# Kernel tuning notes

Hardware: AMD Instinct MI355X
Metric: run time of the kernel (lower is better)

Reference implementation:

```python
import jax, jax.numpy as jnp
import numpy as np
import math

L, B, S, D, H, DI, V = 4, 2, 1024, 768, 12, 3072, 512
DK = D // H

def gelu_tanh(x):
    c = math.sqrt(2.0 / math.pi)
    return 0.5 * x * (1.0 + jnp.tanh(c * (x + 0.044715 * x ** 3)))

def layer_norm(x, g, b, eps=1e-5):
    mu = jnp.mean(x, axis=-1, keepdims=True)
    var = jnp.var(x, axis=-1, keepdims=True)
    return (x - mu) * jax.lax.rsqrt(var + eps) * g + b

def setup_inputs() -> dict:
    key = jax.random.key(0)
    ks = jax.random.split(key, 12)
    w = 0.02  # init scale
    return {
        "x": jax.random.randint(ks[0], (B, S), 0, V),
        "embed": jax.random.normal(ks[1], (V, D), jnp.float32) * w,
        "pos_emb": jax.random.normal(ks[2], (S, D), jnp.float32) * w,
        "ln1_g": jnp.ones((L, D), jnp.float32),
        "ln1_b": jnp.zeros((L, D), jnp.float32),
        "wq": jax.random.normal(ks[3], (L, D, D), jnp.float32) * w,
        "bq": jnp.zeros((L, D), jnp.float32),
        "wk": jax.random.normal(ks[4], (L, D, D), jnp.float32) * w,
        "bk": jnp.zeros((L, D), jnp.float32),
        "wv": jax.random.normal(ks[5], (L, D, D), jnp.float32) * w,
        "bv": jnp.zeros((L, D), jnp.float32),
        "wo": jax.random.normal(ks[6], (L, D, D), jnp.float32) * w,
        "bo": jnp.zeros((L, D), jnp.float32),
        "ln2_g": jnp.ones((L, D), jnp.float32),
        "ln2_b": jnp.zeros((L, D), jnp.float32),
        "w_in": jax.random.normal(ks[7], (L, D, DI), jnp.float32) * w,
        "b_in": jnp.zeros((L, DI), jnp.float32),
        "w_out": jax.random.normal(ks[8], (L, DI, D), jnp.float32) * w,
        "b_out": jnp.zeros((L, D), jnp.float32),
        "lnf_g": jnp.ones((D,), jnp.float32),
        "lnf_b": jnp.zeros((D,), jnp.float32),
        "out_w": jax.random.normal(ks[9], (D, V), jnp.float32) * w,
    }

def reference(x, embed, pos_emb, ln1_g, ln1_b, wq, bq, wk, bk, wv, bv, wo, bo,
              ln2_g, ln2_b, w_in, b_in, w_out, b_out, lnf_g, lnf_b, out_w):
    s = x.shape[1]
    h = embed[x] + pos_emb[None, :s]                       # [B,S,D]
    causal = jnp.tril(jnp.ones((s, s), bool))              # True = keep
    scale = 1.0 / math.sqrt(DK)
    for l in range(L):
        a = layer_norm(h, ln1_g[l], ln1_b[l])
        q = (a @ wq[l] + bq[l]).reshape(-1, s, H, DK)
        k = (a @ wk[l] + bk[l]).reshape(-1, s, H, DK)
        v = (a @ wv[l] + bv[l]).reshape(-1, s, H, DK)
        scores = jnp.einsum('bqhd,bkhd->bhqk', q, k) * scale
        scores = jnp.where(causal, scores, -jnp.inf)
        attn = jax.nn.softmax(scores, axis=-1)
        o = jnp.einsum('bhqk,bkhd->bqhd', attn, v).reshape(-1, s, D)
        h = h + o @ wo[l] + bo[l]
        f = layer_norm(h, ln2_g[l], ln2_b[l])
        h = h + gelu_tanh(f @ w_in[l] + b_in[l]) @ w_out[l] + b_out[l]
    h = layer_norm(h, lnf_g, lnf_b)
    return h @ out_w                                       # [B,S,V] logits
```

## Files before the change

kernel.cpp:

```cpp
#include <hip/hip_runtime.h>
#include <hip/hip_bf16.h>


#define TKN    2048
#define DMODEL 768
#define SEQ    1024
#define NH     12
#define DHEAD  64
#define DFF    3072
#define NL     4
#define NVOCAB 512
#define NQKV   2304

typedef unsigned short u16;
typedef __attribute__((ext_vector_type(4))) float f32x4;
typedef __attribute__((ext_vector_type(8))) short short8;
typedef __attribute__((ext_vector_type(4))) unsigned short us4;

__device__ __forceinline__ u16 f2bf(float f) {
  unsigned u = __builtin_bit_cast(unsigned, f);
  u += 0x7fffu + ((u >> 16) & 1u);
  return (u16)(u >> 16);
}

__device__ __forceinline__ float bf2f(u16 u) {
  unsigned v = ((unsigned)u) << 16;
  return __builtin_bit_cast(float, v);
}

__device__ __forceinline__ short8 mk8(us4 lo, us4 hi) {
  short8 r;
  r[0] = (short)lo[0]; r[1] = (short)lo[1]; r[2] = (short)lo[2]; r[3] = (short)lo[3];
  r[4] = (short)hi[0]; r[5] = (short)hi[1]; r[6] = (short)hi[2]; r[7] = (short)hi[3];
  return r;
}

__device__ __forceinline__ void gload16(const u16* g, u16* l) {
  __builtin_amdgcn_global_load_lds(
      (const __attribute__((address_space(1))) unsigned int*)g,
      (__attribute__((address_space(3))) unsigned int*)l, 16, 0, 0);
}

__global__ __launch_bounds__(256) void k_embed(const int* __restrict__ x,
                                               const float* __restrict__ emb,
                                               const float* __restrict__ pos,
                                               float* __restrict__ h) {
  int t = blockIdx.x;
  int s = t & (SEQ - 1);
  int id = x[t];
  int d = threadIdx.x;
#pragma unroll
  for (int j = 0; j < 3; ++j, d += 256)
    h[t * DMODEL + d] = emb[id * DMODEL + d] + pos[s * DMODEL + d];
}

__global__ __launch_bounds__(256) void k_ln(const float* __restrict__ h,
                                            const float* __restrict__ gam,
                                            const float* __restrict__ bet,
                                            u16* __restrict__ out) {
  __shared__ float sbuf[8];
  int row = blockIdx.x, tid = threadIdx.x;
  const float* hr = h + (size_t)row * DMODEL;
  float x0 = hr[tid], x1 = hr[tid + 256], x2 = hr[tid + 512];
  float s = x0 + x1 + x2;
#pragma unroll
  for (int off = 32; off > 0; off >>= 1) s += __shfl_down(s, off);
  if ((tid & 63) == 0) sbuf[tid >> 6] = s;
  __syncthreads();
  float mu = (sbuf[0] + sbuf[1] + sbuf[2] + sbuf[3]) * (1.0f / DMODEL);
  float d0 = x0 - mu, d1 = x1 - mu, d2 = x2 - mu;
  float v = d0 * d0 + d1 * d1 + d2 * d2;
#pragma unroll
  for (int off = 32; off > 0; off >>= 1) v += __shfl_down(v, off);
  if ((tid & 63) == 0) sbuf[4 + (tid >> 6)] = v;
  __syncthreads();
  float var = (sbuf[4] + sbuf[5] + sbuf[6] + sbuf[7]) * (1.0f / DMODEL);
  float rstd = rsqrtf(var + 1e-5f);
  size_t o = (size_t)row * DMODEL;
  out[o + tid]       = f2bf(d0 * rstd * gam[tid]       + bet[tid]);
  out[o + tid + 256] = f2bf(d1 * rstd * gam[tid + 256] + bet[tid + 256]);
  out[o + tid + 512] = f2bf(d2 * rstd * gam[tid + 512] + bet[tid + 512]);
}

__device__ __forceinline__ void cvt_tile(const float* __restrict__ src, int ldS,
                                         int k0, int n0src,
                                         u16* __restrict__ dst, int ldD, int n0dst,
                                         int tid, u16 (*tl)[72]) {
  int kr = tid >> 2, nj = (tid & 3) << 4;
  const float* sp = src + (size_t)(k0 + kr) * ldS + n0src + nj;
  float4 a0 = ((const float4*)sp)[0];
  float4 a1 = ((const float4*)sp)[1];
  float4 a2 = ((const float4*)sp)[2];
  float4 a3 = ((const float4*)sp)[3];
  u16* tr = &tl[kr][nj];
  tr[0]=f2bf(a0.x); tr[1]=f2bf(a0.y); tr[2]=f2bf(a0.z); tr[3]=f2bf(a0.w);
  tr[4]=f2bf(a1.x); tr[5]=f2bf(a1.y); tr[6]=f2bf(a1.z); tr[7]=f2bf(a1.w);
  tr[8]=f2bf(a2.x); tr[9]=f2bf(a2.y); tr[10]=f2bf(a2.z); tr[11]=f2bf(a2.w);
  tr[12]=f2bf(a3.x); tr[13]=f2bf(a3.y); tr[14]=f2bf(a3.z); tr[15]=f2bf(a3.w);
  __syncthreads();
  int nr = tid >> 2, kj = (tid & 3) << 4;
  us4 o[4];
#pragma unroll
  for (int c = 0; c < 4; ++c)
#pragma unroll
    for (int i = 0; i < 4; ++i) o[c][i] = tl[kj + c * 4 + i][nr];
  u16* dp = dst + (size_t)(n0dst + nr) * ldD + k0 + kj;
  ((us4*)dp)[0] = o[0]; ((us4*)dp)[1] = o[1];
  ((us4*)dp)[2] = o[2]; ((us4*)dp)[3] = o[3];
}

__global__ __launch_bounds__(256) void k_cvtL(const float* __restrict__ wq,
                                              const float* __restrict__ wk,
                                              const float* __restrict__ wv,
                                              const float* __restrict__ wo,
                                              const float* __restrict__ win,
                                              const float* __restrict__ wout,
                                              u16* __restrict__ wqkvT,
                                              u16* __restrict__ woT,
                                              u16* __restrict__ winT,
                                              u16* __restrict__ woutT) {
  __shared__ u16 tl[64][72];
  const int l = blockIdx.y;
  const size_t wDD = (size_t)DMODEL * DMODEL, wDF = (size_t)DMODEL * DFF;
  int t = blockIdx.x, tid = threadIdx.x;
  if (t < 432) {
    int kt = t % 12, ntile = t / 12;
    int gn0 = ntile * 64, sel = gn0 / DMODEL;
    const float* src = (sel == 0 ? wq : sel == 1 ? wk : wv) + l * wDD;
    cvt_tile(src, DMODEL, kt * 64, gn0 - sel * DMODEL,
             wqkvT + l * (size_t)NQKV * DMODEL, DMODEL, gn0, tid, tl);
  } else if (t < 576) {
    int t2 = t - 432, kt = t2 % 12, nt = t2 / 12;
    cvt_tile(wo + l * wDD, DMODEL, kt * 64, nt * 64,
             woT + l * wDD, DMODEL, nt * 64, tid, tl);
  } else if (t < 1152) {
    int t3 = t - 576, kt = t3 % 12, nt = t3 / 12;
    cvt_tile(win + l * wDF, DFF, kt * 64, nt * 64,
             winT + l * wDF, DMODEL, nt * 64, tid, tl);
  } else {
    int t4 = t - 1152, kt = t4 % 48, nt = t4 / 48;
    cvt_tile(wout + l * wDF, DMODEL, kt * 64, nt * 64,
             woutT + l * wDF, DFF, nt * 64, tid, tl);
  }
}

__global__ __launch_bounds__(256) void k_cvtT(const float* __restrict__ src,
                                              u16* __restrict__ dst,
                                              int K, int N) {
  __shared__ u16 tl[64][72];
  cvt_tile(src, N, blockIdx.x * 64, blockIdx.y * 64, dst, K, blockIdx.y * 64,
           threadIdx.x, tl);
}

__global__ __launch_bounds__(256) void k_packb(const float* __restrict__ bq,
                                               const float* __restrict__ bk,
                                               const float* __restrict__ bv,
                                               float* __restrict__ dst) {
  int i = blockIdx.x * 256 + threadIdx.x;
  if (i < NL * NQKV) {
    int l = i / NQKV, j = i - l * NQKV;
    float v = j < DMODEL ? bq[l * DMODEL + j]
            : j < 2 * DMODEL ? bk[l * DMODEL + j - DMODEL]
            : bv[l * DMODEL + j - 2 * DMODEL];
    dst[i] = v;
  }
}

template <int EP, int BM, int BN>
__global__ __launch_bounds__(256) void k_mm(const u16* __restrict__ A,
                                            const u16* __restrict__ BT,
                                            const float* __restrict__ bias,
                                            void* __restrict__ outp,
                                            int N, int K) {
  constexpr int MI = BM / 32;
  constexpr int NJ = BN / 32;
  __shared__ __align__(16) u16 As[2][BM * 64];
  __shared__ __align__(16) u16 Bs[2][BN * 64];
  const int nbx = gridDim.x;
  int lin = blockIdx.y * nbx + blockIdx.x;
  const int chunk = (nbx * gridDim.y) >> 3;
  lin = (lin & 7) * chunk + (lin >> 3);
  const int bn = (lin % nbx) * BN, bm = (lin / nbx) * BM;

  const int tid = threadIdx.x, lane = tid & 63, wid = tid >> 6;
  const int g = lane >> 4, fl = lane & 15;
  const int wm = wid >> 1, wn = wid & 1;

  const int srow = wid * 8 + (lane >> 3);
  const int scol = ((lane & 7) ^ (lane >> 3)) << 3;
  const u16* ag = A + (size_t)(bm + srow) * K + scol;
  const u16* bg = BT + (size_t)(bn + srow) * K + scol;

  f32x4 acc[MI][NJ] = {};
  const int sw = (fl & 7) << 4;

  auto stage = [&](int buf, int kk) {
#pragma unroll
    for (int is = 0; is < MI; ++is)
      gload16(ag + kk + (size_t)is * 32 * K, &As[buf][wid * 512 + is * 2048]);
#pragma unroll
    for (int is = 0; is < NJ; ++is)
      gload16(bg + kk + (size_t)is * 32 * K, &Bs[buf][wid * 512 + is * 2048]);
  };

  const int ks = K / gridDim.z;
  const int kb0 = blockIdx.z * ks;
  const int nk = ks >> 6;
  stage(0, kb0);
  __syncthreads();
  int cur = 0;
  for (int kt = 0; kt < nk; ++kt) {
    if (kt + 1 < nk) stage(cur ^ 1, kb0 + ((kt + 1) << 6));
#pragma unroll
    for (int k0 = 0; k0 < 64; k0 += 32) {
      const int bo = (k0 + 4 * g) * 2;
      short8 af[MI], bf[NJ];
#pragma unroll
      for (int i = 0; i < MI; ++i) {
        const char* base = (const char*)&As[cur][(wm * (BM / 2) + i * 16 + fl) * 64];
        af[i] = mk8(*(const us4*)(base + (bo ^ sw)),
                    *(const us4*)(base + ((bo + 32) ^ sw)));
      }
#pragma unroll
      for (int j = 0; j < NJ; ++j) {
        const char* base = (const char*)&Bs[cur][(wn * (BN / 2) + j * 16 + fl) * 64];
        bf[j] = mk8(*(const us4*)(base + (bo ^ sw)),
                    *(const us4*)(base + ((bo + 32) ^ sw)));
      }
#pragma unroll
      for (int i = 0; i < MI; ++i)
#pragma unroll
        for (int j = 0; j < NJ; ++j)
          acc[i][j] = __builtin_amdgcn_mfma_f32_16x16x32_bf16(af[i], bf[j], acc[i][j], 0, 0, 0);
    }
    __syncthreads();
    cur ^= 1;
  }

  const int row0 = bm + wm * (BM / 2) + 4 * g;
  const int col0 = bn + wn * (BN / 2) + fl;
#pragma unroll
  for (int j = 0; j < NJ; ++j) {
    int col = col0 + j * 16;
    float bv = (EP == 3) ? 0.0f : bias[col];
    if (EP == 1 && blockIdx.z != 0) bv = 0.0f;
#pragma unroll
    for (int i = 0; i < MI; ++i) {
#pragma unroll
      for (int r = 0; r < 4; ++r) {
        int row = row0 + i * 16 + r;
        float val = acc[i][j][r] + bv;
        size_t idx = (size_t)row * N + col;
        if (EP == 0) {
          ((u16*)outp)[idx] = f2bf(val);
        } else if (EP == 1) {
          atomicAdd(&((float*)outp)[idx], val);
        } else if (EP == 2) {
          float t = 0.7978845608028654f * (val + 0.044715f * val * val * val);
          ((u16*)outp)[idx] = f2bf(0.5f * val * (1.0f + tanhf(t)));
        } else if (EP == 3) {
          ((float*)outp)[idx] = val;
        } else {
          int sel = col / DMODEL;
          int c = col - sel * DMODEL;
          int hh2 = c >> 6, dk = c & 63;
          int bb = row >> 10, ss = row & (SEQ - 1);
          if (sel == 0) val *= 0.125f;
          ((u16*)outp)[(size_t)sel * (TKN * DMODEL) +
                       (((size_t)(bb * NH + hh2) * SEQ + ss) << 6) + dk] = f2bf(val);
        }
      }
    }
  }
}

__global__ __launch_bounds__(256) void k_attn(const u16* __restrict__ qh,
                                              u16* __restrict__ pO,
                                              float* __restrict__ pML) {
  __shared__ u16 Vt[DHEAD * 68];
  int bid = blockIdx.x;
  int lin = (bid & 7) * 216 + (bid >> 3);
  const int bh = lin / 72;
  const int idx = lin - bh * 72;
  int qb = 0, sp = 0, c = 0;
#pragma unroll
  for (int q = 0; q < 16; ++q) {
    int n = 1 + (q >> 1);
    if (idx >= c && idx < c + n) { qb = q; sp = idx - c; }
    c += n;
  }
  const int nsp = 1 + (qb >> 1), nt = qb + 1;
  const int t_lo = sp * nt / nsp, t_hi = (sp + 1) * nt / nsp;

  const int b = bh / NH, hh = bh % NH;
  const u16* kh = qh + TKN * DMODEL;
  const u16* vh = qh + 2 * (TKN * DMODEL);
  const size_t headbase = ((size_t)bh * SEQ) << 6;

  const int tid = threadIdx.x, lane = tid & 63, w = tid >> 6;
  const int g = lane >> 4, fl = lane & 15;
  const int qrow = qb * 64 + w * 16 + fl;

  short8 qf[2];
  {
    const u16* qp = qh + headbase + ((size_t)qrow << 6);
#pragma unroll
    for (int hf = 0; hf < 2; ++hf) {
      us4 lo = *(const us4*)(qp + hf * 32 + 4 * g);
      us4 hi = *(const us4*)(qp + hf * 32 + 16 + 4 * g);
      qf[hf] = mk8(lo, hi);
    }
  }

  float m = -1e30f, lsum = 0.0f;
  f32x4 oacc[4] = {};
  const int vr = tid >> 2, vd = (tid & 3) << 4;
  const u16* vbase = vh + headbase + ((size_t)vr << 6) + vd;
  const u16* kbase = kh + headbase;

  {
    const u16* vp = vbase + ((size_t)t_lo << 12);
    us4 vv[4];
#pragma unroll
    for (int qi = 0; qi < 4; ++qi) vv[qi] = *(const us4*)(vp + qi * 4);
#pragma unroll
    for (int qi = 0; qi < 4; ++qi)
#pragma unroll
      for (int i = 0; i < 4; ++i) Vt[(vd + qi * 4 + i) * 68 + vr] = vv[qi][i];
  }
  __syncthreads();

  for (int t64 = t_lo; t64 < t_hi; ++t64) {
    const u16* kb64 = kbase + ((size_t)t64 << 12);
    us4 kv[4][4];
#pragma unroll
    for (int q4 = 0; q4 < 4; ++q4) {
      const u16* kp = kb64 + ((q4 * 16 + fl) << 6);
#pragma unroll
      for (int j = 0; j < 4; ++j) kv[q4][j] = *(const us4*)(kp + j * 16 + 4 * g);
    }
    const bool pf = (t64 + 1 < t_hi);
    us4 vvn[4];
    if (pf) {
      const u16* vp = vbase + ((size_t)(t64 + 1) << 12);
#pragma unroll
      for (int qi = 0; qi < 4; ++qi) vvn[qi] = *(const us4*)(vp + qi * 4);
    }

    f32x4 sfr[4];
    __builtin_amdgcn_s_setprio(1);
#pragma unroll
    for (int sub = 0; sub < 4; ++sub) {
      short8 kf0 = mk8(kv[sub][0], kv[sub][1]);
      short8 kf1 = mk8(kv[sub][2], kv[sub][3]);
      f32x4 s = {};
      s = __builtin_amdgcn_mfma_f32_16x16x32_bf16(kf0, qf[0], s, 0, 0, 0);
      s = __builtin_amdgcn_mfma_f32_16x16x32_bf16(kf1, qf[1], s, 0, 0, 0);
      sfr[sub] = s;
    }
    __builtin_amdgcn_s_setprio(0);

    float sc[16];
    if (t64 == qb) {
#pragma unroll
      for (int sub = 0; sub < 4; ++sub)
#pragma unroll
        for (int r = 0; r < 4; ++r) {
          int key = t64 * 64 + sub * 16 + 4 * g + r;
          sc[sub * 4 + r] = (key <= qrow) ? sfr[sub][r] : -1e30f;
        }
    } else {
#pragma unroll
      for (int sub = 0; sub < 4; ++sub)
#pragma unroll
        for (int r = 0; r < 4; ++r) sc[sub * 4 + r] = sfr[sub][r];
    }
    float pmax = sc[0];
#pragma unroll
    for (int e = 1; e < 16; ++e) pmax = fmaxf(pmax, sc[e]);
    pmax = fmaxf(pmax, __shfl_xor(pmax, 16));
    pmax = fmaxf(pmax, __shfl_xor(pmax, 32));

    float p[16];
    if (__all(pmax <= m + 8.0f)) {
      float ps = 0.0f;
#pragma unroll
      for (int e = 0; e < 16; ++e) { p[e] = __expf(sc[e] - m); ps += p[e]; }
      ps += __shfl_xor(ps, 16);
      ps += __shfl_xor(ps, 32);
      lsum += ps;
    } else {
      float mnew = fmaxf(m, pmax);
      float corr = __expf(m - mnew);
      float ps = 0.0f;
#pragma unroll
      for (int e = 0; e < 16; ++e) { p[e] = __expf(sc[e] - mnew); ps += p[e]; }
      ps += __shfl_xor(ps, 16);
      ps += __shfl_xor(ps, 32);
      lsum = lsum * corr + ps;
      m = mnew;
      float cr[4];
#pragma unroll
      for (int r = 0; r < 4; ++r) cr[r] = __shfl(corr, 4 * g + r);
#pragma unroll
      for (int nb = 0; nb < 4; ++nb)
#pragma unroll
        for (int r = 0; r < 4; ++r) oacc[nb][r] *= cr[r];
    }

    short8 pf0, pf1;
#pragma unroll
    for (int e = 0; e < 8; ++e) { pf0[e] = (short)f2bf(p[e]); pf1[e] = (short)f2bf(p[8 + e]); }

    __builtin_amdgcn_s_setprio(1);
#pragma unroll
    for (int nb = 0; nb < 4; ++nb) {
      const u16* vtp = &Vt[(nb * 16 + fl) * 68 + 4 * g];
      short8 vf0 = mk8(*(const us4*)vtp, *(const us4*)(vtp + 16));
      short8 vf1 = mk8(*(const us4*)(vtp + 32), *(const us4*)(vtp + 48));
      oacc[nb] = __builtin_amdgcn_mfma_f32_16x16x32_bf16(pf0, vf0, oacc[nb], 0, 0, 0);
      oacc[nb] = __builtin_amdgcn_mfma_f32_16x16x32_bf16(pf1, vf1, oacc[nb], 0, 0, 0);
    }
    __builtin_amdgcn_s_setprio(0);

    if (pf) {
      __syncthreads();
#pragma unroll
      for (int qi = 0; qi < 4; ++qi)
#pragma unroll
        for (int i = 0; i < 4; ++i) Vt[(vd + qi * 4 + i) * 68 + vr] = vvn[qi][i];
      __syncthreads();
    }
  }

  const size_t part = ((size_t)bh * 16 + qb) * 8 + sp;
  u16* ob = pO + part * 4096;
  float* ml = pML + part * 128;
#pragma unroll
  for (int nb = 0; nb < 4; ++nb)
#pragma unroll
    for (int r = 0; r < 4; ++r)
      ob[(w * 16 + 4 * g + r) * 64 + nb * 16 + fl] = f2bf(oacc[nb][r]);
  if (g == 0) {
    ml[w * 16 + fl] = m;
    ml[64 + w * 16 + fl] = lsum;
  }
}

__global__ __launch_bounds__(256) void k_ared(const u16* __restrict__ pO,
                                              const float* __restrict__ pML,
                                              u16* __restrict__ O) {
  __shared__ float wgt[8][64];
  __shared__ float iLs[64];
  const int qb = blockIdx.x, bh = blockIdx.y;
  const int nsp = 1 + (qb >> 1);
  const int b = bh / NH, hh = bh % NH;
  const int tid = threadIdx.x;
  const size_t p0 = ((size_t)bh * 16 + qb) * 8;
  if (tid < 64) {
    float M = -1e30f;
    for (int s = 0; s < nsp; ++s) M = fmaxf(M, pML[(p0 + s) * 128 + tid]);
    float L = 0.0f;
    for (int s = 0; s < nsp; ++s) {
      float wv = __expf(pML[(p0 + s) * 128 + tid] - M);
      wgt[s][tid] = wv;
      L += pML[(p0 + s) * 128 + 64 + tid] * wv;
    }
    iLs[tid] = 1.0f / L;
  }
  __syncthreads();
  for (int i = tid; i < 4096; i += 256) {
    int row = i >> 6, d = i & 63;
    float acc = 0.0f;
    for (int s = 0; s < nsp; ++s)
      acc += bf2f(pO[(p0 + s) * 4096 + i]) * wgt[s][row];
    O[(size_t)(b * SEQ + qb * 64 + row) * DMODEL + hh * DHEAD + d] = f2bf(acc * iLs[row]);
  }
}

extern "C" void kernel_launch(void* const* d_in, const int* in_sizes, int n_in,
                              void* d_out, int out_size, void* d_ws, size_t ws_size,
                              hipStream_t stream) {
  const int*   x    = (const int*)d_in[0];
  const float* emb  = (const float*)d_in[1];
  const float* pos  = (const float*)d_in[2];
  const float* ln1g = (const float*)d_in[3];
  const float* ln1b = (const float*)d_in[4];
  const float* wq   = (const float*)d_in[5];
  const float* bq   = (const float*)d_in[6];
  const float* wk   = (const float*)d_in[7];
  const float* bk   = (const float*)d_in[8];
  const float* wv   = (const float*)d_in[9];
  const float* bv   = (const float*)d_in[10];
  const float* wo   = (const float*)d_in[11];
  const float* bo   = (const float*)d_in[12];
  const float* ln2g = (const float*)d_in[13];
  const float* ln2b = (const float*)d_in[14];
  const float* win  = (const float*)d_in[15];
  const float* bin  = (const float*)d_in[16];
  const float* wout = (const float*)d_in[17];
  const float* bout = (const float*)d_in[18];
  const float* lnfg = (const float*)d_in[19];
  const float* lnfb = (const float*)d_in[20];
  const float* outw = (const float*)d_in[21];

  char* w8 = (char*)d_ws;
  float* h    = (float*)(w8);
  u16* abuf   = (u16*)(w8 + 6291456);
  float* pML  = (float*)(w8 + 6291456);
  u16* qkvh   = (u16*)(w8 + 9437184);
  u16* ffbuf  = (u16*)(w8 + 9437184);
  u16* obuf   = (u16*)(w8 + 18874368);
  u16* outwT  = (u16*)(w8 + 22020096);
  float* bqkv = (float*)(w8 + 22806528);
  u16* pO     = (u16*)(w8 + 22843392);
  u16* wqkvT  = (u16*)(w8 + 48009216);
  u16* woT    = (u16*)(w8 + 62164992);
  u16* winT   = (u16*)(w8 + 66883584);
  u16* woutT  = (u16*)(w8 + 85757952);

  const size_t wDD = (size_t)DMODEL * DMODEL, wDF = (size_t)DMODEL * DFF;
  const size_t wQKV = (size_t)NQKV * DMODEL;

  k_embed<<<TKN, 256, 0, stream>>>(x, emb, pos, h);
  k_packb<<<36, 256, 0, stream>>>(bq, bk, bv, bqkv);
  k_cvtT<<<dim3(12, 8), 256, 0, stream>>>(outw, outwT, DMODEL, NVOCAB);
  k_cvtL<<<dim3(1728, NL), 256, 0, stream>>>(wq, wk, wv, wo, win, wout,
                                             wqkvT, woT, winT, woutT);

  for (int l = 0; l < NL; ++l) {
    k_ln<<<TKN, 256, 0, stream>>>(h, ln1g + l * DMODEL, ln1b + l * DMODEL, abuf);
    k_mm<4, 128, 64><<<dim3(NQKV / 64, TKN / 128, 1), 256, 0, stream>>>(
        abuf, wqkvT + l * wQKV, bqkv + l * NQKV, qkvh, NQKV, DMODEL);
    k_attn<<<1728, 256, 0, stream>>>(qkvh, pO, pML);
    k_ared<<<dim3(SEQ / 64, 2 * NH), 256, 0, stream>>>(pO, pML, obuf);
    k_mm<1, 128, 64><<<dim3(DMODEL / 64, TKN / 128, 2), 256, 0, stream>>>(
        obuf, woT + l * wDD, bo + l * DMODEL, h, DMODEL, DMODEL);
    k_ln<<<TKN, 256, 0, stream>>>(h, ln2g + l * DMODEL, ln2b + l * DMODEL, abuf);
    k_mm<2, 128, 64><<<dim3(DFF / 64, TKN / 128, 1), 256, 0, stream>>>(
        abuf, winT + l * wDF, bin + l * DFF, ffbuf, DFF, DMODEL);
    k_mm<1, 128, 64><<<dim3(DMODEL / 64, TKN / 128, 4), 256, 0, stream>>>(
        ffbuf, woutT + l * wDF, bout + l * DMODEL, h, DMODEL, DFF);
  }

  k_ln<<<TKN, 256, 0, stream>>>(h, lnfg, lnfb, abuf);
  k_mm<3, 64, 64><<<dim3(NVOCAB / 64, TKN / 64, 1), 256, 0, stream>>>(
      abuf, outwT, nullptr, d_out, NVOCAB, DMODEL);
}
```

Before: 761.8 us.

## Rework layernorm, weight conversion, GELU epilogue and attention split count

LayerNorm now uses one wavefront per row with float4 loads and xor-shuffle reductions, so it needs no shared memory or block barriers. Weight conversion is merged into a single kernel with larger per-block chunks and no LDS transpose, and it also handles the output projection. The GELU epilogue switches from tanhf to an equivalent sigmoid form using __expf. Attention reduces the number of key splits per query block (max 4 instead of 8), which lowers the block count and the partial-reduce work but may reduce parallelism.

```diff
diff --git a/kernel.cpp b/kernel.cpp
--- a/kernel.cpp
+++ b/kernel.cpp
@@ -16,6 +16,7 @@
 typedef __attribute__((ext_vector_type(4))) float f32x4;
 typedef __attribute__((ext_vector_type(8))) short short8;
 typedef __attribute__((ext_vector_type(4))) unsigned short us4;
+typedef __attribute__((ext_vector_type(8))) unsigned short us8;
 
 __device__ __forceinline__ u16 f2bf(float f) {
   unsigned u = __builtin_bit_cast(unsigned, f);
@@ -58,98 +59,98 @@
                                             const float* __restrict__ gam,
                                             const float* __restrict__ bet,
                                             u16* __restrict__ out) {
-  __shared__ float sbuf[8];
-  int row = blockIdx.x, tid = threadIdx.x;
+  const int w = threadIdx.x >> 6, lane = threadIdx.x & 63;
+  const int row = blockIdx.x * 4 + w;
   const float* hr = h + (size_t)row * DMODEL;
-  float x0 = hr[tid], x1 = hr[tid + 256], x2 = hr[tid + 512];
-  float s = x0 + x1 + x2;
-#pragma unroll
-  for (int off = 32; off > 0; off >>= 1) s += __shfl_down(s, off);
-  if ((tid & 63) == 0) sbuf[tid >> 6] = s;
-  __syncthreads();
-  float mu = (sbuf[0] + sbuf[1] + sbuf[2] + sbuf[3]) * (1.0f / DMODEL);
-  float d0 = x0 - mu, d1 = x1 - mu, d2 = x2 - mu;
-  float v = d0 * d0 + d1 * d1 + d2 * d2;
-#pragma unroll
-  for (int off = 32; off > 0; off >>= 1) v += __shfl_down(v, off);
-  if ((tid & 63) == 0) sbuf[4 + (tid >> 6)] = v;
-  __syncthreads();
-  float var = (sbuf[4] + sbuf[5] + sbuf[6] + sbuf[7]) * (1.0f / DMODEL);
-  float rstd = rsqrtf(var + 1e-5f);
+  float4 v0 = *(const float4*)(hr + lane * 4);
+  float4 v1 = *(const float4*)(hr + 256 + lane * 4);
+  float4 v2 = *(const float4*)(hr + 512 + lane * 4);
+  float s = v0.x + v0.y + v0.z + v0.w + v1.x + v1.y + v1.z + v1.w
+          + v2.x + v2.y + v2.z + v2.w;
+#pragma unroll
+  for (int off = 32; off > 0; off >>= 1) s += __shfl_xor(s, off);
+  float mu = s * (1.0f / DMODEL);
+  float d[12] = {v0.x - mu, v0.y - mu, v0.z - mu, v0.w - mu,
+                 v1.x - mu, v1.y - mu, v1.z - mu, v1.w - mu,
+                 v2.x - mu, v2.y - mu, v2.z - mu, v2.w - mu};
+  float q = 0.0f;
+#pragma unroll
+  for (int i = 0; i < 12; ++i) q += d[i] * d[i];
+#pragma unroll
+  for (int off = 32; off > 0; off >>= 1) q += __shfl_xor(q, off);
+  float rstd = rsqrtf(q * (1.0f / DMODEL) + 1e-5f);
   size_t o = (size_t)row * DMODEL;
-  out[o + tid]       = f2bf(d0 * rstd * gam[tid]       + bet[tid]);
-  out[o + tid + 256] = f2bf(d1 * rstd * gam[tid + 256] + bet[tid + 256]);
-  out[o + tid + 512] = f2bf(d2 * rstd * gam[tid + 512] + bet[tid + 512]);
-}
-
-__device__ __forceinline__ void cvt_tile(const float* __restrict__ src, int ldS,
-                                         int k0, int n0src,
-                                         u16* __restrict__ dst, int ldD, int n0dst,
-                                         int tid, u16 (*tl)[72]) {
-  int kr = tid >> 2, nj = (tid & 3) << 4;
-  const float* sp = src + (size_t)(k0 + kr) * ldS + n0src + nj;
-  float4 a0 = ((const float4*)sp)[0];
-  float4 a1 = ((const float4*)sp)[1];
-  float4 a2 = ((const float4*)sp)[2];
-  float4 a3 = ((const float4*)sp)[3];
-  u16* tr = &tl[kr][nj];
-  tr[0]=f2bf(a0.x); tr[1]=f2bf(a0.y); tr[2]=f2bf(a0.z); tr[3]=f2bf(a0.w);
-  tr[4]=f2bf(a1.x); tr[5]=f2bf(a1.y); tr[6]=f2bf(a1.z); tr[7]=f2bf(a1.w);
-  tr[8]=f2bf(a2.x); tr[9]=f2bf(a2.y); tr[10]=f2bf(a2.z); tr[11]=f2bf(a2.w);
-  tr[12]=f2bf(a3.x); tr[13]=f2bf(a3.y); tr[14]=f2bf(a3.z); tr[15]=f2bf(a3.w);
-  __syncthreads();
-  int nr = tid >> 2, kj = (tid & 3) << 4;
-  us4 o[4];
-#pragma unroll
-  for (int c = 0; c < 4; ++c)
-#pragma unroll
-    for (int i = 0; i < 4; ++i) o[c][i] = tl[kj + c * 4 + i][nr];
-  u16* dp = dst + (size_t)(n0dst + nr) * ldD + k0 + kj;
-  ((us4*)dp)[0] = o[0]; ((us4*)dp)[1] = o[1];
-  ((us4*)dp)[2] = o[2]; ((us4*)dp)[3] = o[3];
-}
-
-__global__ __launch_bounds__(256) void k_cvtL(const float* __restrict__ wq,
+#pragma unroll
+  for (int j = 0; j < 3; ++j) {
+    float4 gv = *(const float4*)(gam + j * 256 + lane * 4);
+    float4 bv = *(const float4*)(bet + j * 256 + lane * 4);
+    us4 ov;
+    ov[0] = f2bf(d[j * 4 + 0] * rstd * gv.x + bv.x);
+    ov[1] = f2bf(d[j * 4 + 1] * rstd * gv.y + bv.y);
+    ov[2] = f2bf(d[j * 4 + 2] * rstd * gv.z + bv.z);
+    ov[3] = f2bf(d[j * 4 + 3] * rstd * gv.w + bv.w);
+    *(us4*)(out + o + j * 256 + lane * 4) = ov;
+  }
+}
+
+__global__ __launch_bounds__(256) void k_cvtW(const float* __restrict__ wq,
                                               const float* __restrict__ wk,
                                               const float* __restrict__ wv,
                                               const float* __restrict__ wo,
                                               const float* __restrict__ win,
                                               const float* __restrict__ wout,
+                                              const float* __restrict__ outw,
                                               u16* __restrict__ wqkvT,
                                               u16* __restrict__ woT,
                                               u16* __restrict__ winT,
-                                              u16* __restrict__ woutT) {
-  __shared__ u16 tl[64][72];
+                                              u16* __restrict__ woutT,
+                                              u16* __restrict__ outwT) {
   const int l = blockIdx.y;
+  const int t = blockIdx.x;
   const size_t wDD = (size_t)DMODEL * DMODEL, wDF = (size_t)DMODEL * DFF;
-  int t = blockIdx.x, tid = threadIdx.x;
-  if (t < 432) {
-    int kt = t % 12, ntile = t / 12;
-    int gn0 = ntile * 64, sel = gn0 / DMODEL;
-    const float* src = (sel == 0 ? wq : sel == 1 ? wk : wv) + l * wDD;
-    cvt_tile(src, DMODEL, kt * 64, gn0 - sel * DMODEL,
-             wqkvT + l * (size_t)NQKV * DMODEL, DMODEL, gn0, tid, tl);
-  } else if (t < 576) {
-    int t2 = t - 432, kt = t2 % 12, nt = t2 / 12;
-    cvt_tile(wo + l * wDD, DMODEL, kt * 64, nt * 64,
-             woT + l * wDD, DMODEL, nt * 64, tid, tl);
-  } else if (t < 1152) {
-    int t3 = t - 576, kt = t3 % 12, nt = t3 / 12;
-    cvt_tile(win + l * wDF, DFF, kt * 64, nt * 64,
-             winT + l * wDF, DMODEL, nt * 64, tid, tl);
+  const float* src; u16* dst;
+  int ldS, ldD, scol0, n0, k0;
+  if (t < 72) {
+    int ntile = t >> 1, kc = t & 1;
+    int gn0 = ntile * 64, sel = ntile / 12;
+    src = (sel == 0 ? wq : sel == 1 ? wk : wv) + l * wDD; ldS = DMODEL;
+    dst = wqkvT + l * (size_t)NQKV * DMODEL; ldD = DMODEL;
+    scol0 = gn0 - sel * DMODEL; n0 = gn0; k0 = kc * 384;
+  } else if (t < 96) {
+    int t2 = t - 72, ntile = t2 >> 1, kc = t2 & 1;
+    src = wo + l * wDD; ldS = DMODEL;
+    dst = woT + l * wDD; ldD = DMODEL;
+    scol0 = ntile * 64; n0 = ntile * 64; k0 = kc * 384;
+  } else if (t < 192) {
+    int t3 = t - 96, ntile = t3 >> 1, kc = t3 & 1;
+    src = win + l * wDF; ldS = DFF;
+    dst = winT + l * wDF; ldD = DMODEL;
+    scol0 = ntile * 64; n0 = ntile * 64; k0 = kc * 384;
+  } else if (t < 288) {
+    int t4 = t - 192, ntile = t4 >> 3, kc = t4 & 7;
+    src = wout + l * wDF; ldS = DMODEL;
+    dst = woutT + l * wDF; ldD = DFF;
+    scol0 = ntile * 64; n0 = ntile * 64; k0 = kc * 384;
   } else {
-    int t4 = t - 1152, kt = t4 % 48, nt = t4 / 48;
-    cvt_tile(wout + l * wDF, DMODEL, kt * 64, nt * 64,
-             woutT + l * wDF, DFF, nt * 64, tid, tl);
-  }
-}
-
-__global__ __launch_bounds__(256) void k_cvtT(const float* __restrict__ src,
-                                              u16* __restrict__ dst,
-                                              int K, int N) {
-  __shared__ u16 tl[64][72];
-  cvt_tile(src, N, blockIdx.x * 64, blockIdx.y * 64, dst, K, blockIdx.y * 64,
-           threadIdx.x, tl);
+    if (l != 0) return;
+    int t5 = t - 288, ntile = t5 >> 1, kc = t5 & 1;
+    src = outw; ldS = NVOCAB;
+    dst = outwT; ldD = DMODEL;
+    scol0 = ntile * 64; n0 = ntile * 64; k0 = kc * 384;
+  }
+  const int lane = threadIdx.x & 63, w = threadIdx.x >> 6;
+  const float* sp = src + (size_t)(k0 + w * 96) * ldS + scol0 + lane;
+  u16* dp = dst + (size_t)(n0 + lane) * ldD + k0 + w * 96;
+#pragma unroll
+  for (int c = 0; c < 3; ++c) {
+    u16 ob[32];
+#pragma unroll
+    for (int k = 0; k < 32; ++k)
+      ob[k] = f2bf(sp[(size_t)(c * 32 + k) * ldS]);
+#pragma unroll
+    for (int q = 0; q < 4; ++q)
+      *(us8*)(dp + c * 32 + q * 8) = *(us8*)&ob[q * 8];
+  }
 }
 
 __global__ __launch_bounds__(256) void k_packb(const float* __restrict__ bq,
@@ -256,8 +257,8 @@
         } else if (EP == 1) {
           atomicAdd(&((float*)outp)[idx], val);
         } else if (EP == 2) {
-          float t = 0.7978845608028654f * (val + 0.044715f * val * val * val);
-          ((u16*)outp)[idx] = f2bf(0.5f * val * (1.0f + tanhf(t)));
+          float t = 1.5957691216057308f * (val + 0.044715f * val * val * val);
+          ((u16*)outp)[idx] = f2bf(val / (1.0f + __expf(-t)));
         } else if (EP == 3) {
           ((float*)outp)[idx] = val;
         } else {
@@ -279,17 +280,15 @@
                                               float* __restrict__ pML) {
   __shared__ u16 Vt[DHEAD * 68];
   int bid = blockIdx.x;
-  int lin = (bid & 7) * 216 + (bid >> 3);
-  const int bh = lin / 72;
-  const int idx = lin - bh * 72;
-  int qb = 0, sp = 0, c = 0;
-#pragma unroll
-  for (int q = 0; q < 16; ++q) {
-    int n = 1 + (q >> 1);
-    if (idx >= c && idx < c + n) { qb = q; sp = idx - c; }
-    c += n;
-  }
-  const int nsp = 1 + (qb >> 1), nt = qb + 1;
+  int lin = (bid & 7) * 120 + (bid >> 3);
+  const int bh = lin / 40;
+  const int idx = lin - bh * 40;
+  int qb, sp;
+  if (idx < 4)       { qb = idx;                     sp = 0; }
+  else if (idx < 12) { qb = 4 + ((idx - 4) >> 1);    sp = (idx - 4) & 1; }
+  else if (idx < 24) { int t = idx - 12; qb = 8 + t / 3;  sp = t - (t / 3) * 3; }
+  else               { int t = idx - 24; qb = 12 + (t >> 2); sp = t & 3; }
+  const int nsp = 1 + (qb >> 2), nt = qb + 1;
   const int t_lo = sp * nt / nsp, t_hi = (sp + 1) * nt / nsp;
 
   const int b = bh / NH, hh = bh % NH;
@@ -433,7 +432,7 @@
     }
   }
 
-  const size_t part = ((size_t)bh * 16 + qb) * 8 + sp;
+  const size_t part = ((size_t)bh * 16 + qb) * 4 + sp;
   u16* ob = pO + part * 4096;
   float* ml = pML + part * 128;
 #pragma unroll
@@ -450,13 +449,13 @@
 __global__ __launch_bounds__(256) void k_ared(const u16* __restrict__ pO,
                                               const float* __restrict__ pML,
                                               u16* __restrict__ O) {
-  __shared__ float wgt[8][64];
+  __shared__ float wgt[4][64];
   __shared__ float iLs[64];
   const int qb = blockIdx.x, bh = blockIdx.y;
-  const int nsp = 1 + (qb >> 1);
+  const int nsp = 1 + (qb >> 2);
   const int b = bh / NH, hh = bh % NH;
   const int tid = threadIdx.x;
-  const size_t p0 = ((size_t)bh * 16 + qb) * 8;
+  const size_t p0 = ((size_t)bh * 16 + qb) * 4;
   if (tid < 64) {
     float M = -1e30f;
     for (int s = 0; s < nsp; ++s) M = fmaxf(M, pML[(p0 + s) * 128 + tid]);
@@ -524,26 +523,25 @@
 
   k_embed<<<TKN, 256, 0, stream>>>(x, emb, pos, h);
   k_packb<<<36, 256, 0, stream>>>(bq, bk, bv, bqkv);
-  k_cvtT<<<dim3(12, 8), 256, 0, stream>>>(outw, outwT, DMODEL, NVOCAB);
-  k_cvtL<<<dim3(1728, NL), 256, 0, stream>>>(wq, wk, wv, wo, win, wout,
-                                             wqkvT, woT, winT, woutT);
+  k_cvtW<<<dim3(304, NL), 256, 0, stream>>>(wq, wk, wv, wo, win, wout, outw,
+                                            wqkvT, woT, winT, woutT, outwT);
 
   for (int l = 0; l < NL; ++l) {
-    k_ln<<<TKN, 256, 0, stream>>>(h, ln1g + l * DMODEL, ln1b + l * DMODEL, abuf);
+    k_ln<<<TKN / 4, 256, 0, stream>>>(h, ln1g + l * DMODEL, ln1b + l * DMODEL, abuf);
     k_mm<4, 128, 64><<<dim3(NQKV / 64, TKN / 128, 1), 256, 0, stream>>>(
         abuf, wqkvT + l * wQKV, bqkv + l * NQKV, qkvh, NQKV, DMODEL);
-    k_attn<<<1728, 256, 0, stream>>>(qkvh, pO, pML);
+    k_attn<<<960, 256, 0, stream>>>(qkvh, pO, pML);
     k_ared<<<dim3(SEQ / 64, 2 * NH), 256, 0, stream>>>(pO, pML, obuf);
     k_mm<1, 128, 64><<<dim3(DMODEL / 64, TKN / 128, 2), 256, 0, stream>>>(
         obuf, woT + l * wDD, bo + l * DMODEL, h, DMODEL, DMODEL);
-    k_ln<<<TKN, 256, 0, stream>>>(h, ln2g + l * DMODEL, ln2b + l * DMODEL, abuf);
+    k_ln<<<TKN / 4, 256, 0, stream>>>(h, ln2g + l * DMODEL, ln2b + l * DMODEL, abuf);
     k_mm<2, 128, 64><<<dim3(DFF / 64, TKN / 128, 1), 256, 0, stream>>>(
         abuf, winT + l * wDF, bin + l * DFF, ffbuf, DFF, DMODEL);
     k_mm<1, 128, 64><<<dim3(DMODEL / 64, TKN / 128, 4), 256, 0, stream>>>(
         ffbuf, woutT + l * wDF, bout + l * DMODEL, h, DMODEL, DFF);
   }
 
-  k_ln<<<TKN, 256, 0, stream>>>(h, lnfg, lnfb, abuf);
+  k_ln<<<TKN / 4, 256, 0, stream>>>(h, lnfg, lnfb, abuf);
   k_mm<3, 64, 64><<<dim3(NVOCAB / 64, TKN / 64, 1), 256, 0, stream>>>(
       abuf, outwT, nullptr, d_out, NVOCAB, DMODEL);
 }
```

New measurement: 693.8 us. 8.9% less time.
